# Optimization experiments

Measured on AMD Instinct MI355X. Metric: run time of the kernel, lower is better.

The kernel has to match this reference:

```python
import jax, jax.numpy as jnp
import numpy as np

B, S, DIM, HEADS, HD, FF = 2, 2048, 1024, 16, 64, 4096
PREV, MAX_SEQ, THETA, POS_BIAS_MAX, EPS = 1024, 4096, 10000.0, 2.0, 1e-6


def _freqs_cos_sin():
    inv = 1.0 / THETA ** (np.arange(0, HD, 2)[: HD // 2].astype(np.float32) / HD)
    f = np.outer(np.arange(MAX_SEQ, dtype=np.float32), inv)
    return jnp.asarray(np.cos(f), jnp.float32), jnp.asarray(np.sin(f), jnp.float32)


def setup_inputs():
    key = jax.random.key(0)
    ks = jax.random.split(key, 16)
    lin = lambda k, o, i: 0.02 * jax.random.normal(k, (o, i), jnp.float32)
    cos, sin = _freqs_cos_sin()
    return {
        "x": jax.random.normal(ks[0], (B, S, DIM), jnp.float32),
        "cache_k": jax.random.normal(ks[1], (B, HEADS, PREV, HD), jnp.float32),
        "cache_v": jax.random.normal(ks[2], (B, HEADS, PREV, HD), jnp.float32),
        "cos": cos, "sin": sin,
        "attn_norm_w": jnp.ones((DIM,), jnp.float32),
        "ffn_norm_w": jnp.ones((DIM,), jnp.float32),
        "wq": lin(ks[3], DIM, DIM), "bq": jnp.zeros((DIM,), jnp.float32),
        "wk": lin(ks[4], DIM, DIM), "bk": jnp.zeros((DIM,), jnp.float32),
        "wv": lin(ks[5], DIM, DIM), "bv": jnp.zeros((DIM,), jnp.float32),
        "wo": lin(ks[6], DIM, DIM), "bo": jnp.zeros((DIM,), jnp.float32),
        "w_gate": lin(ks[7], FF, DIM), "b_gate": jnp.zeros((FF,), jnp.float32),
        "w_value": lin(ks[8], FF, DIM), "b_value": jnp.zeros((FF,), jnp.float32),
        "w_proj": lin(ks[9], DIM, FF), "b_proj": jnp.zeros((DIM,), jnp.float32),
        "cache_limit": 3072,
    }


def _rmsnorm(h, w):
    return h * jax.lax.rsqrt(jnp.mean(h * h, axis=-1, keepdims=True) + EPS) * w


def _rope(t, cos, sin):
    # t: [B,H,L,HD]; cos/sin: [L, HD//2]; rotate interleaved pairs (complex mult)
    t2 = t.reshape(t.shape[:-1] + (HD // 2, 2))
    x0, x1 = t2[..., 0], t2[..., 1]
    c = cos[None, None]
    s = sin[None, None]
    out = jnp.stack([x0 * c - x1 * s, x0 * s + x1 * c], axis=-1)
    return out.reshape(t.shape)


def _forward(x, cache_k, cache_v, cos, sin, attn_norm_w, ffn_norm_w, wq, bq, wk, bk, wv, bv, wo, bo, w_gate, b_gate, w_value, b_value, w_proj, b_proj, cache_limit):
    b, s, d = x.shape
    h = _rmsnorm(x, attn_norm_w)
    shape4 = lambda t: t.reshape(b, s, HEADS, HD).transpose(0, 2, 1, 3)  # [B,H,S,HD]
    q = shape4(h @ wq.T + bq)
    k_new = shape4(h @ wk.T + bk)
    v_new = shape4(h @ wv.T + bv)
    k_all = jnp.concatenate([cache_k, k_new], axis=2)
    v_all = jnp.concatenate([cache_v, v_new], axis=2)
    if cache_limit > 0:
        k_all = k_all[:, :, -cache_limit:, :]
        v_all = v_all[:, :, -cache_limit:, :]
    total = k_all.shape[2]
    prev = total - s
    # RoPE: q at absolute positions prev..prev+s-1, keys at 0..total-1 (mod cache len)
    pos_q = (jnp.arange(s) + prev) % MAX_SEQ
    pos_k = jnp.arange(total) % MAX_SEQ
    q = _rope(q, cos[pos_q], sin[pos_q])
    k = _rope(k_all, cos[pos_k], sin[pos_k])
    # linear positional bias + causal mask over the new-token block only
    slope = POS_BIAS_MAX / max(total - 1, 1)
    j = jnp.arange(total, dtype=jnp.float32)[None, :]
    i_abs = (prev + jnp.arange(s, dtype=jnp.float32))[:, None]
    bias = slope * (j - i_abs)  # [s, total]
    causal = (jnp.arange(total)[None, :] - prev) > jnp.arange(s)[:, None]
    mask = jnp.where(causal, -jnp.inf, bias)
    scores = jnp.einsum('bhsd,bhtd->bhst', q, k) / jnp.sqrt(jnp.float32(HD)) + mask
    attn = jax.nn.softmax(scores, axis=-1)
    ctx = jnp.einsum('bhst,bhtd->bhsd', attn, v_all)
    ctx = ctx.transpose(0, 2, 1, 3).reshape(b, s, d)
    x = x + ctx @ wo.T + bo
    h2 = _rmsnorm(x, ffn_norm_w)
    gated = jax.nn.silu(h2 @ w_gate.T + b_gate) * (h2 @ w_value.T + b_value)
    return x + gated @ w_proj.T + b_proj


def reference(x, cache_k, cache_v, cos, sin, attn_norm_w, ffn_norm_w, wq, bq, wk, bk, wv, bv, wo, bo, w_gate, b_gate, w_value, b_value, w_proj, b_proj, cache_limit):
    return _forward(x, cache_k, cache_v, cos, sin, attn_norm_w, ffn_norm_w, wq, bq, wk, bk, wv, bv, wo, bo, w_gate, b_gate, w_value, b_value, w_proj, b_proj, cache_limit)
```

## Files before the change

kernel.cpp:

```cpp
#include <hip/hip_runtime.h>
#include <stdint.h>

typedef unsigned short u16;
typedef unsigned int   u32;
typedef __bf16 bf16x8 __attribute__((ext_vector_type(8)));
typedef float  f32x4  __attribute__((ext_vector_type(4)));
typedef u32    u32x4  __attribute__((ext_vector_type(4)));
typedef u32    u32x2  __attribute__((ext_vector_type(2)));

#define B_SZ  2
#define S_LEN 2048
#define NH    16
#define HD    64
#define DIM   1024
#define FF    4096
#define T_LEN 3072
#define PREV  1024
#define MROWS (B_SZ * S_LEN)
#define LOG2E 1.44269504f

#define MFMA16 __builtin_amdgcn_mfma_f32_16x16x32_bf16

__device__ __forceinline__ u16 f2bf(float f) {
  u32 u = __builtin_bit_cast(u32, f);
  u32 r = u + 0x7FFFu + ((u >> 16) & 1u);
  return (u16)(r >> 16);
}
__device__ __forceinline__ float bf2f(u16 h) {
  u32 u = ((u32)h) << 16;
  return __builtin_bit_cast(float, u);
}
__device__ __forceinline__ u32 cvtpk(float lo, float hi) {
  u32 r;
  asm("v_cvt_pk_bf16_f32 %0, %1, %2" : "=v"(r) : "v"(lo), "v"(hi));
  return r;
}

__device__ __forceinline__ void gl_lds16(const void* g, void* l) {
  __builtin_amdgcn_global_load_lds(
      (const __attribute__((address_space(1))) u32*)g,
      (__attribute__((address_space(3))) u32*)l, 16, 0, 0);
}

__global__ __launch_bounds__(256) void cvt_kernel(const float* __restrict__ src,
                                                  u16* __restrict__ dst, int n4) {
  int i = blockIdx.x * 256 + threadIdx.x;
  const int stride = gridDim.x * 256;
  for (; i < n4; i += stride) {
    f32x4 v = *(const f32x4*)&src[(long)i * 4];
    u32x2 o;
    o[0] = (u32)f2bf(v[0]) | ((u32)f2bf(v[1]) << 16);
    o[1] = (u32)f2bf(v[2]) | ((u32)f2bf(v[3]) << 16);
    *(u32x2*)&dst[(long)i * 4] = o;
  }
}

__global__ __launch_bounds__(256) void cvt_ilv_kernel(const float* __restrict__ wg,
                                                      const float* __restrict__ wval,
                                                      u16* __restrict__ dst) {
  int i = blockIdx.x * 256 + threadIdx.x;
  const int stride = gridDim.x * 256;
  const int upr = DIM / 4;
  for (; i < FF * upr; i += stride) {
    int j = i / upr;
    int c = (i - j * upr) * 4;
    f32x4 g = *(const f32x4*)&wg[(long)j * DIM + c];
    f32x4 v = *(const f32x4*)&wval[(long)j * DIM + c];
    u32x2 og, ov;
    og[0] = (u32)f2bf(g[0]) | ((u32)f2bf(g[1]) << 16);
    og[1] = (u32)f2bf(g[2]) | ((u32)f2bf(g[3]) << 16);
    ov[0] = (u32)f2bf(v[0]) | ((u32)f2bf(v[1]) << 16);
    ov[1] = (u32)f2bf(v[2]) | ((u32)f2bf(v[3]) << 16);
    *(u32x2*)&dst[((long)2 * j) * DIM + c] = og;
    *(u32x2*)&dst[((long)2 * j + 1) * DIM + c] = ov;
  }
}

__global__ __launch_bounds__(256) void bias_ilv_kernel(const float* __restrict__ bg,
                                                       const float* __restrict__ bval,
                                                       float* __restrict__ dst) {
  int i = blockIdx.x * 256 + threadIdx.x;
  if (i < FF) {
    dst[2 * i] = bg[i];
    dst[2 * i + 1] = bval[i];
  }
}

__global__ __launch_bounds__(256) void rmsnorm_kernel(const float* __restrict__ x,
                                                      const float* __restrict__ w,
                                                      u16* __restrict__ out) {
  const int row = blockIdx.x;
  const int tid = threadIdx.x;
  const long base = (long)row * DIM + tid * 4;
  f32x4 v = *(const f32x4*)&x[base];
  float ss = v[0] * v[0] + v[1] * v[1] + v[2] * v[2] + v[3] * v[3];
#pragma unroll
  for (int d = 1; d <= 32; d <<= 1) ss += __shfl_xor(ss, d, 64);
  __shared__ float red[4];
  if ((tid & 63) == 0) red[tid >> 6] = ss;
  __syncthreads();
  float tot = red[0] + red[1] + red[2] + red[3];
  const float sc = rsqrtf(tot * (1.f / (float)DIM) + 1e-6f);
  f32x4 wv4 = *(const f32x4*)&w[tid * 4];
  u32x2 o;
  o[0] = (u32)f2bf(v[0] * sc * wv4[0]) | ((u32)f2bf(v[1] * sc * wv4[1]) << 16);
  o[1] = (u32)f2bf(v[2] * sc * wv4[2]) | ((u32)f2bf(v[3] * sc * wv4[3]) << 16);
  *(u32x2*)&out[base] = o;
}

template <int EPI, int NB>
__global__ __launch_bounds__(256) void gemm_bt(const u16* __restrict__ A,
                                               const u16* __restrict__ Bw,
                                               const float* __restrict__ bias,
                                               const float* __restrict__ resid,
                                               u16* __restrict__ out_bf,
                                               float* __restrict__ out_f,
                                               int N, int K) {
  constexpr int BHALF = NB / 64;
  constexpr int NFR = NB / 32;
  constexpr int LPT = 2 + BHALF;
  __shared__ __align__(16) u16 As[3][128 * 32];
  __shared__ __align__(16) u16 Bs[3][NB * 32];
  const int tid = threadIdx.x;
  const int lane = tid & 63;
  const int wv = tid >> 6;
  const int wr = wv >> 1, wc = wv & 1;
  const long m0 = (long)blockIdx.y * 128;
  const long n0 = (long)blockIdx.x * NB;

  const int arow = tid >> 2;
  const int acol = (tid & 3) << 3;
  const u16* ag = A + (m0 + arow) * K + acol;
  const u16* bg = Bw + (n0 + arow) * K + acol;
  const long hK = (long)64 * K;

  f32x4 acc[4][NFR] = {};
  const int l15 = lane & 15;
  const int lhi = lane >> 4;
  const int aoff0 = (wr * 64 + l15) * 32 + lhi * 8;
  const int boff0 = (wc * (NB / 2) + l15) * 32 + lhi * 8;
  const int nk = K >> 5;

  auto stage = [&](int t, int buf) {
    const int k0 = t << 5;
    gl_lds16(ag + k0, &As[buf][tid * 8]);
    gl_lds16(ag + k0 + hK, &As[buf][2048 + tid * 8]);
    gl_lds16(bg + k0, &Bs[buf][tid * 8]);
    if (BHALF == 2) gl_lds16(bg + k0 + hK, &Bs[buf][2048 + tid * 8]);
  };

  stage(0, 0);
  stage(1, 1);
  asm volatile("s_waitcnt vmcnt(%0)" ::"n"(LPT) : "memory");
  __builtin_amdgcn_s_barrier();
  asm volatile("" ::: "memory");
  __builtin_amdgcn_sched_barrier(0);

  for (int t = 0; t < nk; ++t) {
    const int cb = t % 3;
    if (t + 2 < nk) stage(t + 2, (t + 2) % 3);
    bf16x8 af[4], bfr[NFR];
#pragma unroll
    for (int i = 0; i < 4; ++i) af[i] = *(const bf16x8*)&As[cb][aoff0 + i * 16 * 32];
#pragma unroll
    for (int j = 0; j < NFR; ++j) bfr[j] = *(const bf16x8*)&Bs[cb][boff0 + j * 16 * 32];
    __builtin_amdgcn_s_setprio(1);
#pragma unroll
    for (int i = 0; i < 4; ++i)
#pragma unroll
      for (int j = 0; j < NFR; ++j)
        acc[i][j] = MFMA16(af[i], bfr[j], acc[i][j], 0, 0, 0);
    __builtin_amdgcn_s_setprio(0);
    if (t + 2 < nk) {
      asm volatile("s_waitcnt vmcnt(%0)" ::"n"(LPT) : "memory");
      __builtin_amdgcn_s_barrier();
      asm volatile("" ::: "memory");
      __builtin_amdgcn_sched_barrier(0);
    } else if (t + 1 < nk) {
      asm volatile("s_waitcnt vmcnt(0)" ::: "memory");
      __builtin_amdgcn_s_barrier();
      asm volatile("" ::: "memory");
      __builtin_amdgcn_sched_barrier(0);
    }
  }

#pragma unroll
  for (int i = 0; i < 4; ++i) {
    const long row0 = m0 + wr * 64 + i * 16 + lhi * 4;
#pragma unroll
    for (int j = 0; j < NFR; ++j) {
      const long col = n0 + wc * (NB / 2) + j * 16 + l15;
      const float bb = bias[col];
#pragma unroll
      for (int r = 0; r < 4; ++r) {
        float v = acc[i][j][r] + bb;
        if (EPI == 2) {
          float other = __shfl_xor(v, 1, 64);
          if (!(l15 & 1)) {
            float s = v / (1.f + __expf(-v)) * other;
            out_bf[(row0 + r) * (N >> 1) + (col >> 1)] = f2bf(s);
          }
        } else {
          const long idx = (row0 + r) * N + col;
          if (EPI == 0) out_bf[idx] = f2bf(v);
          else          out_f[idx] = resid[idx] + v;
        }
      }
    }
  }
}

__global__ __launch_bounds__(256) void rope_q_kernel(const u16* __restrict__ qkv,
                                                     const float* __restrict__ cosT,
                                                     const float* __restrict__ sinT,
                                                     u16* __restrict__ Q) {
  int idx = blockIdx.x * 256 + threadIdx.x;
  int u = idx & 7;
  int s = (idx >> 3) & (S_LEN - 1);
  int bh = idx >> 14;
  int b = bh >> 4, h = bh & 15;
  int pos = PREV + s;
  const float SC = 0.125f * LOG2E;
  const u16* src = qkv + ((long)(b * S_LEN + s)) * (3 * DIM) + h * HD + u * 8;
  u32x4 d = *(const u32x4*)src;
  f32x4 cv = *(const f32x4*)&cosT[(long)pos * 32 + u * 4];
  f32x4 sv = *(const f32x4*)&sinT[(long)pos * 32 + u * 4];
  u32x4 o;
#pragma unroll
  for (int p = 0; p < 4; ++p) {
    float x0 = bf2f((u16)(d[p] & 0xffff));
    float x1 = bf2f((u16)(d[p] >> 16));
    float y0 = (x0 * cv[p] - x1 * sv[p]) * SC;
    float y1 = (x0 * sv[p] + x1 * cv[p]) * SC;
    o[p] = (u32)f2bf(y0) | ((u32)f2bf(y1) << 16);
  }
  *(u32x4*)&Q[((long)bh * S_LEN + s) * HD + u * 8] = o;
}

__global__ __launch_bounds__(256) void rope_k_kernel(const u16* __restrict__ qkv,
                                                     const float* __restrict__ cache_k,
                                                     const float* __restrict__ cosT,
                                                     const float* __restrict__ sinT,
                                                     u16* __restrict__ Kall) {
  int idx = blockIdx.x * 256 + threadIdx.x;
  int u = idx & 7;
  int t2 = idx >> 3;
  int j = t2 % T_LEN;
  int bh = t2 / T_LEN;
  int b = bh >> 4, h = bh & 15;
  float e[8];
  if (j < PREV) {
    const float* src = cache_k + ((long)bh * PREV + j) * HD + u * 8;
    f32x4 a = *(const f32x4*)src;
    f32x4 c = *(const f32x4*)(src + 4);
    e[0] = a[0]; e[1] = a[1]; e[2] = a[2]; e[3] = a[3];
    e[4] = c[0]; e[5] = c[1]; e[6] = c[2]; e[7] = c[3];
  } else {
    const u16* src = qkv + ((long)(b * S_LEN + (j - PREV))) * (3 * DIM) + DIM + h * HD + u * 8;
    u32x4 d = *(const u32x4*)src;
#pragma unroll
    for (int p = 0; p < 4; ++p) {
      e[2 * p] = bf2f((u16)(d[p] & 0xffff));
      e[2 * p + 1] = bf2f((u16)(d[p] >> 16));
    }
  }
  f32x4 cv = *(const f32x4*)&cosT[(long)j * 32 + u * 4];
  f32x4 sv = *(const f32x4*)&sinT[(long)j * 32 + u * 4];
  u32x4 o;
#pragma unroll
  for (int p = 0; p < 4; ++p) {
    float y0 = e[2 * p] * cv[p] - e[2 * p + 1] * sv[p];
    float y1 = e[2 * p] * sv[p] + e[2 * p + 1] * cv[p];
    o[p] = (u32)f2bf(y0) | ((u32)f2bf(y1) << 16);
  }
  *(u32x4*)&Kall[((long)bh * T_LEN + j) * HD + (u ^ (j & 7)) * 8] = o;
}

__global__ __launch_bounds__(256) void build_vt_kernel(const u16* __restrict__ qkv,
                                                       const float* __restrict__ cache_v,
                                                       u16* __restrict__ Vtg) {
  int idx = blockIdx.x * 256 + threadIdx.x;
  int hd = idx & 63;
  int t2 = idx >> 6;
  int kb = t2 % 384;
  int bh = t2 / 384;
  int b = bh >> 4, h = bh & 15;
  int key0 = kb * 8;
  u16 vals[8];
  if (key0 < PREV) {
#pragma unroll
    for (int i = 0; i < 8; ++i)
      vals[i] = f2bf(cache_v[((long)bh * PREV + key0 + i) * HD + hd]);
  } else {
#pragma unroll
    for (int i = 0; i < 8; ++i)
      vals[i] = qkv[((long)(b * S_LEN + key0 + i - PREV)) * (3 * DIM) + 2 * DIM + h * HD + hd];
  }
  u32x4 o;
#pragma unroll
  for (int p = 0; p < 4; ++p)
    o[p] = (u32)vals[2 * p] | ((u32)vals[2 * p + 1] << 16);
  const int span = kb >> 3;
  const int u = (kb & 7) ^ (hd & 7);
  *(u32x4*)&Vtg[((long)bh * HD + hd) * T_LEN + span * 64 + u * 8] = o;
}

__global__ __launch_bounds__(256, 4) void attn_kernel(const u16* __restrict__ Q,
                                                      const u16* __restrict__ Kg,
                                                      const u16* __restrict__ Vtg,
                                                      u16* __restrict__ ctx, float slope2) {
  __shared__ __align__(16) u16 Ks[2][64 * 64];
  __shared__ __align__(16) u16 Vs[2][64 * 64];
  __shared__ __align__(16) u16 Ps[4][16 * 64];

  const int tid = threadIdx.x;
  const int lane = tid & 63;
  const int wv = tid >> 6;
  const int l15 = lane & 15;
  const int lhi = lane >> 4;
  const int c7 = l15 & 7;
  const int bh = blockIdx.x;
  const int qt = blockIdx.y;
  const int b = bh >> 4, h = bh & 15;
  const int q0 = qt * 64;
  const int nt = (PREV + q0 + 64) >> 6;

  const long qrow = (long)bh * S_LEN + q0 + wv * 16 + l15;
  bf16x8 aq0 = *(const bf16x8*)&Q[qrow * HD + lhi * 8];
  bf16x8 aq1 = *(const bf16x8*)&Q[qrow * HD + 32 + lhi * 8];

  const long kgb = (long)bh * T_LEN * HD;
  const long vgb = (long)bh * HD * T_LEN;
  const int srow = tid >> 3;
  const int sunit = (tid & 7) * 8;

  gl_lds16(&Kg[kgb + (long)srow * HD + sunit], &Ks[0][tid * 8]);
  gl_lds16(&Kg[kgb + (long)(srow + 32) * HD + sunit], &Ks[0][2048 + tid * 8]);
  gl_lds16(&Vtg[vgb + (long)srow * T_LEN + sunit], &Vs[0][tid * 8]);
  gl_lds16(&Vtg[vgb + (long)(srow + 32) * T_LEN + sunit], &Vs[0][2048 + tid * 8]);
  __syncthreads();

  f32x4 o[4] = {};
  float mrun = -1e30f, lrun = 0.f;
  const int iabs = PREV + q0 + wv * 16 + l15;
  u16* Pw = &Ps[wv][0];

  for (int t = 0; t < nt; ++t) {
    const int cur = t & 1, nxt = cur ^ 1;
    const int kt0 = t << 6;
    if (t + 1 < nt) {
      const int kn = kt0 + 64;
      gl_lds16(&Kg[kgb + (long)(kn + srow) * HD + sunit], &Ks[nxt][tid * 8]);
      gl_lds16(&Kg[kgb + (long)(kn + srow + 32) * HD + sunit], &Ks[nxt][2048 + tid * 8]);
      gl_lds16(&Vtg[vgb + (long)srow * T_LEN + kn + sunit], &Vs[nxt][tid * 8]);
      gl_lds16(&Vtg[vgb + (long)(srow + 32) * T_LEN + kn + sunit], &Vs[nxt][2048 + tid * 8]);
    }

    f32x4 sf[4];
    __builtin_amdgcn_s_setprio(1);
#pragma unroll
    for (int jf = 0; jf < 4; ++jf) {
      const int krow = jf * 16 + l15;
      bf16x8 ak0 = *(const bf16x8*)&Ks[cur][krow * 64 + ((lhi ^ c7) * 8)];
      bf16x8 ak1 = *(const bf16x8*)&Ks[cur][krow * 64 + (((4 + lhi) ^ c7) * 8)];
      f32x4 s = {};
      s = MFMA16(ak0, aq0, s, 0, 0, 0);
      s = MFMA16(ak1, aq1, s, 0, 0, 0);
      sf[jf] = s;
    }
    __builtin_amdgcn_s_setprio(0);

    const bool masked = (t == nt - 1);
#pragma unroll
    for (int jf = 0; jf < 4; ++jf)
#pragma unroll
      for (int r = 0; r < 4; ++r) {
        const int jcol = kt0 + jf * 16 + 4 * lhi + r;
        float s_ = sf[jf][r] + slope2 * (float)(jcol - iabs);
        sf[jf][r] = (masked && jcol > iabs) ? -1e30f : s_;
      }

    float t0 = fmaxf(fmaxf(sf[0][0], sf[0][1]), fmaxf(sf[0][2], sf[0][3]));
    float t1 = fmaxf(fmaxf(sf[1][0], sf[1][1]), fmaxf(sf[1][2], sf[1][3]));
    float t2 = fmaxf(fmaxf(sf[2][0], sf[2][1]), fmaxf(sf[2][2], sf[2][3]));
    float t3 = fmaxf(fmaxf(sf[3][0], sf[3][1]), fmaxf(sf[3][2], sf[3][3]));
    float pmax = fmaxf(fmaxf(t0, t1), fmaxf(t2, t3));
    pmax = fmaxf(pmax, __shfl_xor(pmax, 16, 64));
    pmax = fmaxf(pmax, __shfl_xor(pmax, 32, 64));

    if (!__all(pmax - mrun <= 8.f)) {
      float mnew = fmaxf(mrun, pmax);
      float scl = exp2f(mrun - mnew);
      mrun = mnew;
      lrun *= scl;
#pragma unroll
      for (int r = 0; r < 4; ++r) {
        float sr = __shfl(scl, 4 * lhi + r, 64);
#pragma unroll
        for (int hf = 0; hf < 4; ++hf) o[hf][r] *= sr;
      }
    }

    float ps = 0.f;
#pragma unroll
    for (int jf = 0; jf < 4; ++jf) {
      f32x4 p;
#pragma unroll
      for (int r = 0; r < 4; ++r) {
        p[r] = exp2f(sf[jf][r] - mrun);
        ps += p[r];
      }
      u32x2 pw2;
      pw2[0] = cvtpk(p[0], p[1]);
      pw2[1] = cvtpk(p[2], p[3]);
      const int u = (2 * jf + (lhi >> 1)) ^ c7;
      *(u32x2*)&Pw[l15 * 64 + u * 8 + (lhi & 1) * 4] = pw2;
    }
    ps += __shfl_xor(ps, 16, 64);
    ps += __shfl_xor(ps, 32, 64);
    lrun += ps;

    bf16x8 pa0 = *(const bf16x8*)&Pw[l15 * 64 + ((lhi ^ c7) * 8)];
    bf16x8 pa1 = *(const bf16x8*)&Pw[l15 * 64 + (((4 + lhi) ^ c7) * 8)];
    __builtin_amdgcn_s_setprio(1);
#pragma unroll
    for (int hf = 0; hf < 4; ++hf) {
      const int vrow = hf * 16 + l15;
      bf16x8 bv0 = *(const bf16x8*)&Vs[cur][vrow * 64 + ((lhi ^ c7) * 8)];
      bf16x8 bv1 = *(const bf16x8*)&Vs[cur][vrow * 64 + (((4 + lhi) ^ c7) * 8)];
      o[hf] = MFMA16(pa0, bv0, o[hf], 0, 0, 0);
      o[hf] = MFMA16(pa1, bv1, o[hf], 0, 0, 0);
    }
    __builtin_amdgcn_s_setprio(0);
    __syncthreads();
  }

#pragma unroll
  for (int r = 0; r < 4; ++r) {
    const float inv = 1.f / __shfl(lrun, 4 * lhi + r, 64);
    const long srow_ = (long)b * S_LEN + q0 + wv * 16 + 4 * lhi + r;
#pragma unroll
    for (int hf = 0; hf < 4; ++hf)
      ctx[srow_ * DIM + h * HD + hf * 16 + l15] = f2bf(o[hf][r] * inv);
  }
}

extern "C" void kernel_launch(void* const* d_in, const int* in_sizes, int n_in,
                              void* d_out, int out_size, void* d_ws, size_t ws_size,
                              hipStream_t stream) {
  (void)in_sizes; (void)n_in; (void)out_size; (void)ws_size;
  const float* x       = (const float*)d_in[0];
  const float* cache_k = (const float*)d_in[1];
  const float* cache_v = (const float*)d_in[2];
  const float* cosT    = (const float*)d_in[3];
  const float* sinT    = (const float*)d_in[4];
  const float* attn_w  = (const float*)d_in[5];
  const float* ffn_w   = (const float*)d_in[6];
  const float* wq      = (const float*)d_in[7];
  const float* bq      = (const float*)d_in[8];
  const float* wk      = (const float*)d_in[9];
  const float* bk      = (const float*)d_in[10];
  const float* wv_     = (const float*)d_in[11];
  const float* bv      = (const float*)d_in[12];
  const float* wo      = (const float*)d_in[13];
  const float* bo      = (const float*)d_in[14];
  const float* wg      = (const float*)d_in[15];
  const float* bg      = (const float*)d_in[16];
  const float* wval    = (const float*)d_in[17];
  const float* bval    = (const float*)d_in[18];
  const float* wp      = (const float*)d_in[19];
  const float* bp      = (const float*)d_in[20];
  float* out = (float*)d_out;

  char* w = (char*)d_ws;
  size_t off = 0;
  auto alloc = [&](size_t bytes) -> char* {
    char* p = w + off;
    off += (bytes + 255) & ~(size_t)255;
    return p;
  };
  u16*   wqkv_bf  = (u16*)alloc((size_t)3 * DIM * DIM * 2);
  u16*   wo_bf    = (u16*)alloc((size_t)DIM * DIM * 2);
  u16*   wgv_bf   = (u16*)alloc((size_t)2 * FF * DIM * 2);
  u16*   wproj_bf = (u16*)alloc((size_t)DIM * FF * 2);
  float* bqkv     = (float*)alloc((size_t)3 * DIM * 4);
  float* bgv      = (float*)alloc((size_t)2 * FF * 4);
  float* x2       = (float*)alloc((size_t)MROWS * DIM * 4);
  char* AR = alloc((size_t)117440512);
  u16* qkv   = (u16*)(AR + 0);
  u16* Qb    = (u16*)(AR + 25165824);
  u16* Kb    = (u16*)(AR + 33554432);
  u16* Vtg   = (u16*)(AR + 46137344);
  u16* h1    = (u16*)(AR + 58720256);
  u16* ctx   = (u16*)(AR + 0);
  u16* h2    = (u16*)(AR + 8388608);
  u16* gated = (u16*)(AR + 16777216);

  cvt_kernel<<<512, 256, 0, stream>>>(wq, wqkv_bf, DIM * DIM / 4);
  cvt_kernel<<<512, 256, 0, stream>>>(wk, wqkv_bf + DIM * DIM, DIM * DIM / 4);
  cvt_kernel<<<512, 256, 0, stream>>>(wv_, wqkv_bf + 2 * DIM * DIM, DIM * DIM / 4);
  cvt_kernel<<<512, 256, 0, stream>>>(wo, wo_bf, DIM * DIM / 4);
  cvt_ilv_kernel<<<1024, 256, 0, stream>>>(wg, wval, wgv_bf);
  cvt_kernel<<<1024, 256, 0, stream>>>(wp, wproj_bf, DIM * FF / 4);
  bias_ilv_kernel<<<16, 256, 0, stream>>>(bg, bval, bgv);
  hipMemcpyAsync(bqkv, bq, DIM * 4, hipMemcpyDeviceToDevice, stream);
  hipMemcpyAsync(bqkv + DIM, bk, DIM * 4, hipMemcpyDeviceToDevice, stream);
  hipMemcpyAsync(bqkv + 2 * DIM, bv, DIM * 4, hipMemcpyDeviceToDevice, stream);

  rmsnorm_kernel<<<MROWS, 256, 0, stream>>>(x, attn_w, h1);
  gemm_bt<0, 128><<<dim3(24, 32), 256, 0, stream>>>(h1, wqkv_bf, bqkv, nullptr, qkv,
                                                    nullptr, 3 * DIM, DIM);
  rope_q_kernel<<<2048, 256, 0, stream>>>(qkv, cosT, sinT, Qb);
  rope_k_kernel<<<3072, 256, 0, stream>>>(qkv, cache_k, cosT, sinT, Kb);
  build_vt_kernel<<<3072, 256, 0, stream>>>(qkv, cache_v, Vtg);
  attn_kernel<<<dim3(B_SZ * NH, S_LEN / 64), 256, 0, stream>>>(
      Qb, Kb, Vtg, ctx, (2.0f / (float)(T_LEN - 1)) * LOG2E);
  gemm_bt<1, 64><<<dim3(16, 32), 256, 0, stream>>>(ctx, wo_bf, bo, x, nullptr, x2,
                                                   DIM, DIM);
  rmsnorm_kernel<<<MROWS, 256, 0, stream>>>(x2, ffn_w, h2);
  gemm_bt<2, 128><<<dim3(64, 32), 256, 0, stream>>>(h2, wgv_bf, bgv, nullptr, gated,
                                                    nullptr, 2 * FF, DIM);
  gemm_bt<1, 64><<<dim3(16, 32), 256, 0, stream>>>(gated, wproj_bf, bp, x2, nullptr, out,
                                                   DIM, FF);
}
```

Before: 397.7 us.

## Add 256x256 tiled GEMM with XOR-swizzled operands for QKV and gate/value projections

Introduces a 512-thread GEMM kernel with 256x256 output tiles, a K-step of 64 and double-buffered LDS. It replaces the 128-wide GEMMs for the QKV and fused gate/value projections. To avoid LDS bank conflicts, the A operands (rmsnorm outputs) and B operands (weight conversions) are written in an XOR-swizzled 16-byte-unit layout, and the fragment reads undo the swizzle. The larger tiles raise data reuse per load, at the cost of more registers and LDS per block, fewer blocks in flight, and a more fragile interleaved barrier schedule.

```diff
diff --git a/kernel.cpp b/kernel.cpp
--- a/kernel.cpp
+++ b/kernel.cpp
@@ -42,6 +42,14 @@
       (__attribute__((address_space(3))) u32*)l, 16, 0, 0);
 }
 
+#define GFENCE() asm volatile("" ::: "memory")
+#define BARF()                         \
+  do {                                 \
+    GFENCE();                          \
+    __builtin_amdgcn_s_barrier();      \
+    GFENCE();                          \
+  } while (0)
+
 __global__ __launch_bounds__(256) void cvt_kernel(const float* __restrict__ src,
                                                   u16* __restrict__ dst, int n4) {
   int i = blockIdx.x * 256 + threadIdx.x;
@@ -55,24 +63,55 @@
   }
 }
 
-__global__ __launch_bounds__(256) void cvt_ilv_kernel(const float* __restrict__ wg,
-                                                      const float* __restrict__ wval,
-                                                      u16* __restrict__ dst) {
+__global__ __launch_bounds__(256) void cvt_sw_kernel(const float* __restrict__ src,
+                                                     u16* __restrict__ dst, int nunits) {
   int i = blockIdx.x * 256 + threadIdx.x;
   const int stride = gridDim.x * 256;
-  const int upr = DIM / 4;
-  for (; i < FF * upr; i += stride) {
-    int j = i / upr;
-    int c = (i - j * upr) * 4;
-    f32x4 g = *(const f32x4*)&wg[(long)j * DIM + c];
-    f32x4 v = *(const f32x4*)&wval[(long)j * DIM + c];
-    u32x2 og, ov;
-    og[0] = (u32)f2bf(g[0]) | ((u32)f2bf(g[1]) << 16);
-    og[1] = (u32)f2bf(g[2]) | ((u32)f2bf(g[3]) << 16);
-    ov[0] = (u32)f2bf(v[0]) | ((u32)f2bf(v[1]) << 16);
-    ov[1] = (u32)f2bf(v[2]) | ((u32)f2bf(v[3]) << 16);
-    *(u32x2*)&dst[((long)2 * j) * DIM + c] = og;
-    *(u32x2*)&dst[((long)2 * j + 1) * DIM + c] = ov;
+  for (; i < nunits; i += stride) {
+    int row = i >> 7;
+    int g = i & 127;
+    const float* s = &src[((long)row << 10) + g * 8];
+    f32x4 a = *(const f32x4*)s;
+    f32x4 b = *(const f32x4*)(s + 4);
+    u32x4 o;
+    o[0] = (u32)f2bf(a[0]) | ((u32)f2bf(a[1]) << 16);
+    o[1] = (u32)f2bf(a[2]) | ((u32)f2bf(a[3]) << 16);
+    o[2] = (u32)f2bf(b[0]) | ((u32)f2bf(b[1]) << 16);
+    o[3] = (u32)f2bf(b[2]) | ((u32)f2bf(b[3]) << 16);
+    const int gp = (g & ~7) | ((g & 7) ^ (row & 7));
+    *(u32x4*)&dst[((long)row << 10) + gp * 8] = o;
+  }
+}
+
+__global__ __launch_bounds__(256) void cvt_ilv_sw_kernel(const float* __restrict__ wg,
+                                                         const float* __restrict__ wval,
+                                                         u16* __restrict__ dst) {
+  int i = blockIdx.x * 256 + threadIdx.x;
+  const int stride = gridDim.x * 256;
+  for (; i < FF * 128; i += stride) {
+    int j = i >> 7;
+    int g = i & 127;
+    const float* sg = &wg[((long)j << 10) + g * 8];
+    const float* sv = &wval[((long)j << 10) + g * 8];
+    f32x4 a = *(const f32x4*)sg;
+    f32x4 b = *(const f32x4*)(sg + 4);
+    u32x4 og;
+    og[0] = (u32)f2bf(a[0]) | ((u32)f2bf(a[1]) << 16);
+    og[1] = (u32)f2bf(a[2]) | ((u32)f2bf(a[3]) << 16);
+    og[2] = (u32)f2bf(b[0]) | ((u32)f2bf(b[1]) << 16);
+    og[3] = (u32)f2bf(b[2]) | ((u32)f2bf(b[3]) << 16);
+    f32x4 c = *(const f32x4*)sv;
+    f32x4 d = *(const f32x4*)(sv + 4);
+    u32x4 ov;
+    ov[0] = (u32)f2bf(c[0]) | ((u32)f2bf(c[1]) << 16);
+    ov[1] = (u32)f2bf(c[2]) | ((u32)f2bf(c[3]) << 16);
+    ov[2] = (u32)f2bf(d[0]) | ((u32)f2bf(d[1]) << 16);
+    ov[3] = (u32)f2bf(d[2]) | ((u32)f2bf(d[3]) << 16);
+    const int rg = 2 * j, rv = 2 * j + 1;
+    const int gpg = (g & ~7) | ((g & 7) ^ (rg & 7));
+    const int gpv = (g & ~7) | ((g & 7) ^ (rv & 7));
+    *(u32x4*)&dst[((long)rg << 10) + gpg * 8] = og;
+    *(u32x4*)&dst[((long)rv << 10) + gpv * 8] = ov;
   }
 }
 
@@ -105,7 +144,149 @@
   u32x2 o;
   o[0] = (u32)f2bf(v[0] * sc * wv4[0]) | ((u32)f2bf(v[1] * sc * wv4[1]) << 16);
   o[1] = (u32)f2bf(v[2] * sc * wv4[2]) | ((u32)f2bf(v[3] * sc * wv4[3]) << 16);
-  *(u32x2*)&out[base] = o;
+  const int u = tid >> 1, hf = tid & 1;
+  const int up = (u & 0x78) | ((u & 7) ^ (row & 7));
+  *(u32x2*)&out[(long)row * DIM + up * 8 + hf * 4] = o;
+}
+
+template <int EPI>
+__global__ __launch_bounds__(512, 2) void gemm256(const u16* __restrict__ A,
+                                                  const u16* __restrict__ Bw,
+                                                  const float* __restrict__ bias,
+                                                  u16* __restrict__ out_bf,
+                                                  int N, int K) {
+  __shared__ __align__(16) u16 Ab[2][256 * 64];
+  __shared__ __align__(16) u16 Bb[2][256 * 64];
+  const int tid = threadIdx.x;
+  const int lane = tid & 63;
+  const int wid = tid >> 6;
+  const int wm = wid >> 2, wn = wid & 3;
+  const int l15 = lane & 15, lhi = lane >> 4;
+  const int c7 = l15 & 7;
+  const long m0 = (long)blockIdx.y * 256;
+  const long n0 = (long)blockIdx.x * 256;
+  const int NT = K >> 6;
+
+  const int srow = tid >> 3;
+  const int sunit = (tid & 7) * 8;
+  const u16* agp = A + (m0 + srow) * K + sunit;
+  const u16* bgp = Bw + (n0 + srow) * K + sunit;
+  const int ldst = tid * 8;
+
+  auto stageA = [&](int kt, int b) {
+    const int k0 = kt << 6;
+    u16* d = &Ab[b][0];
+#pragma unroll
+    for (int c = 0; c < 4; ++c)
+      gl_lds16(agp + (long)(c * 64) * K + k0, d + c * 4096 + ldst);
+  };
+  auto stageB = [&](int kt, int b) {
+    const int k0 = kt << 6;
+    u16* d = &Bb[b][0];
+#pragma unroll
+    for (int c = 0; c < 4; ++c)
+      gl_lds16(bgp + (long)(c * 64) * K + k0, d + c * 4096 + ldst);
+  };
+
+#define READ_A(MH)                                                               \
+  _Pragma("unroll") for (int m_ = 0; m_ < 4; ++m_) {                             \
+    _Pragma("unroll") for (int ks_ = 0; ks_ < 2; ++ks_) {                        \
+      Afr[MH][m_ * 2 + ks_] =                                                    \
+          *(const bf16x8*)&Ac[(wm * 128 + (MH)*64 + m_ * 16 + l15) * 64 +        \
+                              (((ks_ * 4 + lhi) ^ c7) * 8)];                     \
+    }                                                                            \
+  }
+#define READ_B(NH)                                                               \
+  _Pragma("unroll") for (int n_ = 0; n_ < 2; ++n_) {                             \
+    _Pragma("unroll") for (int ks_ = 0; ks_ < 2; ++ks_) {                        \
+      Bfr[NH][n_ * 2 + ks_] =                                                    \
+          *(const bf16x8*)&Bc[(wn * 64 + (NH)*32 + n_ * 16 + l15) * 64 +         \
+                              (((ks_ * 4 + lhi) ^ c7) * 8)];                     \
+    }                                                                            \
+  }
+#define QUAD(MH, NH)                                                             \
+  do {                                                                           \
+    __builtin_amdgcn_s_setprio(1);                                               \
+    _Pragma("unroll") for (int m_ = 0; m_ < 4; ++m_) {                           \
+      _Pragma("unroll") for (int n_ = 0; n_ < 2; ++n_) {                         \
+        acc[(MH)*4 + m_][(NH)*2 + n_] =                                          \
+            MFMA16(Afr[MH][m_ * 2], Bfr[NH][n_ * 2],                             \
+                   acc[(MH)*4 + m_][(NH)*2 + n_], 0, 0, 0);                      \
+        acc[(MH)*4 + m_][(NH)*2 + n_] =                                          \
+            MFMA16(Afr[MH][m_ * 2 + 1], Bfr[NH][n_ * 2 + 1],                     \
+                   acc[(MH)*4 + m_][(NH)*2 + n_], 0, 0, 0);                      \
+      }                                                                          \
+    }                                                                            \
+    __builtin_amdgcn_s_setprio(0);                                               \
+  } while (0)
+
+  f32x4 acc[8][4] = {};
+
+  stageA(0, 0);
+  stageB(0, 0);
+  stageA(1, 1);
+  stageB(1, 1);
+  asm volatile("s_waitcnt vmcnt(8)" ::: "memory");
+  __builtin_amdgcn_s_barrier();
+  GFENCE();
+
+  for (int kt = 0; kt < NT; ++kt) {
+    const int b = kt & 1;
+    const u16* Ac = &Ab[b][0];
+    const u16* Bc = &Bb[b][0];
+    bf16x8 Afr[2][8], Bfr[2][4];
+    READ_A(0);
+    READ_B(0);
+    BARF();
+    QUAD(0, 0);
+    BARF();
+    READ_A(1);
+    READ_B(1);
+    BARF();
+    QUAD(0, 1);
+    BARF();
+    if (kt + 2 < NT) stageA(kt + 2, b);
+    BARF();
+    QUAD(1, 0);
+    BARF();
+    if (kt + 2 < NT) stageB(kt + 2, b);
+    BARF();
+    QUAD(1, 1);
+    if (kt + 1 < NT) {
+      if (kt + 2 < NT)
+        asm volatile("s_waitcnt vmcnt(8)" ::: "memory");
+      else
+        asm volatile("s_waitcnt vmcnt(0)" ::: "memory");
+      __builtin_amdgcn_s_barrier();
+      GFENCE();
+    }
+  }
+#undef READ_A
+#undef READ_B
+#undef QUAD
+
+#pragma unroll
+  for (int mi = 0; mi < 8; ++mi) {
+    const long row0 = m0 + wm * 128 + mi * 16 + lhi * 4;
+#pragma unroll
+    for (int ni = 0; ni < 4; ++ni) {
+      const long col = n0 + wn * 64 + ni * 16 + l15;
+      const float bb = bias[col];
+#pragma unroll
+      for (int r = 0; r < 4; ++r) {
+        float v = acc[mi][ni][r] + bb;
+        if (EPI == 2) {
+          float other = __shfl_xor(v, 1, 64);
+          if (!(l15 & 1)) {
+            float s = v / (1.f + __expf(-v)) * other;
+            out_bf[(row0 + r) * (N >> 1) + (col >> 1)] = f2bf(s);
+          }
+        } else {
+          out_bf[(row0 + r) * N + col] = f2bf(v);
+        }
+      }
+    }
+  }
 }
 
 template <int EPI, int NB>
@@ -153,8 +334,7 @@
   stage(1, 1);
   asm volatile("s_waitcnt vmcnt(%0)" ::"n"(LPT) : "memory");
   __builtin_amdgcn_s_barrier();
-  asm volatile("" ::: "memory");
-  __builtin_amdgcn_sched_barrier(0);
+  GFENCE();
 
   for (int t = 0; t < nk; ++t) {
     const int cb = t % 3;
@@ -174,13 +354,11 @@
     if (t + 2 < nk) {
       asm volatile("s_waitcnt vmcnt(%0)" ::"n"(LPT) : "memory");
       __builtin_amdgcn_s_barrier();
-      asm volatile("" ::: "memory");
-      __builtin_amdgcn_sched_barrier(0);
+      GFENCE();
     } else if (t + 1 < nk) {
       asm volatile("s_waitcnt vmcnt(0)" ::: "memory");
       __builtin_amdgcn_s_barrier();
-      asm volatile("" ::: "memory");
-      __builtin_amdgcn_sched_barrier(0);
+      GFENCE();
     }
   }
 
@@ -193,18 +371,10 @@
       const float bb = bias[col];
 #pragma unroll
       for (int r = 0; r < 4; ++r) {
+        const long idx = (row0 + r) * N + col;
         float v = acc[i][j][r] + bb;
-        if (EPI == 2) {
-          float other = __shfl_xor(v, 1, 64);
-          if (!(l15 & 1)) {
-            float s = v / (1.f + __expf(-v)) * other;
-            out_bf[(row0 + r) * (N >> 1) + (col >> 1)] = f2bf(s);
-          }
-        } else {
-          const long idx = (row0 + r) * N + col;
-          if (EPI == 0) out_bf[idx] = f2bf(v);
-          else          out_f[idx] = resid[idx] + v;
-        }
+        if (EPI == 0) out_bf[idx] = f2bf(v);
+        else          out_f[idx] = resid[idx] + v;
       }
     }
   }
@@ -496,11 +666,11 @@
   u16* h2    = (u16*)(AR + 8388608);
   u16* gated = (u16*)(AR + 16777216);
 
-  cvt_kernel<<<512, 256, 0, stream>>>(wq, wqkv_bf, DIM * DIM / 4);
-  cvt_kernel<<<512, 256, 0, stream>>>(wk, wqkv_bf + DIM * DIM, DIM * DIM / 4);
-  cvt_kernel<<<512, 256, 0, stream>>>(wv_, wqkv_bf + 2 * DIM * DIM, DIM * DIM / 4);
+  cvt_sw_kernel<<<512, 256, 0, stream>>>(wq, wqkv_bf, DIM * DIM / 8);
+  cvt_sw_kernel<<<512, 256, 0, stream>>>(wk, wqkv_bf + DIM * DIM, DIM * DIM / 8);
+  cvt_sw_kernel<<<512, 256, 0, stream>>>(wv_, wqkv_bf + 2 * DIM * DIM, DIM * DIM / 8);
   cvt_kernel<<<512, 256, 0, stream>>>(wo, wo_bf, DIM * DIM / 4);
-  cvt_ilv_kernel<<<1024, 256, 0, stream>>>(wg, wval, wgv_bf);
+  cvt_ilv_sw_kernel<<<1024, 256, 0, stream>>>(wg, wval, wgv_bf);
   cvt_kernel<<<1024, 256, 0, stream>>>(wp, wproj_bf, DIM * FF / 4);
   bias_ilv_kernel<<<16, 256, 0, stream>>>(bg, bval, bgv);
   hipMemcpyAsync(bqkv, bq, DIM * 4, hipMemcpyDeviceToDevice, stream);
@@ -508,8 +678,7 @@
   hipMemcpyAsync(bqkv + 2 * DIM, bv, DIM * 4, hipMemcpyDeviceToDevice, stream);
 
   rmsnorm_kernel<<<MROWS, 256, 0, stream>>>(x, attn_w, h1);
-  gemm_bt<0, 128><<<dim3(24, 32), 256, 0, stream>>>(h1, wqkv_bf, bqkv, nullptr, qkv,
-                                                    nullptr, 3 * DIM, DIM);
+  gemm256<0><<<dim3(12, 16), 512, 0, stream>>>(h1, wqkv_bf, bqkv, qkv, 3 * DIM, DIM);
   rope_q_kernel<<<2048, 256, 0, stream>>>(qkv, cosT, sinT, Qb);
   rope_k_kernel<<<3072, 256, 0, stream>>>(qkv, cache_k, cosT, sinT, Kb);
   build_vt_kernel<<<3072, 256, 0, stream>>>(qkv, cache_v, Vtg);
@@ -518,8 +687,7 @@
   gemm_bt<1, 64><<<dim3(16, 32), 256, 0, stream>>>(ctx, wo_bf, bo, x, nullptr, x2,
                                                    DIM, DIM);
   rmsnorm_kernel<<<MROWS, 256, 0, stream>>>(x2, ffn_w, h2);
-  gemm_bt<2, 128><<<dim3(64, 32), 256, 0, stream>>>(h2, wgv_bf, bgv, nullptr, gated,
-                                                    nullptr, 2 * FF, DIM);
+  gemm256<2><<<dim3(32, 16), 512, 0, stream>>>(h2, wgv_bf, bgv, gated, 2 * FF, DIM);
   gemm_bt<1, 64><<<dim3(16, 32), 256, 0, stream>>>(gated, wproj_bf, bp, x2, nullptr, out,
                                                    DIM, FF);
 }
```

Measured after the change: 386.9 us. -2.7%, faster.
